# Kernel optimization log

Hardware: AMD Instinct MI355X
Metric: run time of the kernel (lower is better)

The kernel has to match this reference:

```python
import jax, jax.numpy as jnp
import numpy as np


def hadamard(D):
    # Sylvester Hadamard: H[i,j] = (-1)^popcount(i & j), normalized by sqrt(D)
    x = np.arange(D)[:, None] & np.arange(D)[None, :]
    par = np.zeros_like(x)
    for _ in range(int(np.log2(D)) + 1):
        par ^= x & 1
        x >>= 1
    return ((1.0 - 2.0 * par) / np.sqrt(D)).astype(np.float32)


def setup_inputs() -> dict:
    key = jax.random.key(0)
    ks = jax.random.split(key, 6)
    K, M, D, T = 4, 32, 2048, 128
    z = jax.random.normal(ks[0], (K, M, D, T), dtype=jnp.float32)
    d1 = jax.random.normal(ks[1], (D, 1), dtype=jnp.float32)
    d2 = jax.random.normal(ks[2], (D, 1), dtype=jnp.float32)
    d3 = jax.random.normal(ks[3], (D, 1), dtype=jnp.float32)
    b = jax.random.normal(ks[4], (D, 1), dtype=jnp.float32)
    sldj = jax.random.normal(ks[5], (K * M,), dtype=jnp.float32)
    return {"z": z, "d1": d1, "d2": d2, "d3": d3, "b": b,
            "sum_log_det_jacobians": sldj}


def reference(z, d1, d2, d3, b, sum_log_det_jacobians):
    K, M, D, T = z.shape
    H = jnp.asarray(hadamard(D), dtype=z.dtype)
    # A = H @ D3 @ H @ D2 @ H @ D1
    #   H @ diag(d)  == H * d.T (scale columns)
    #   diag(d) @ X  == d * X   (scale rows)
    A = H @ (d3 * (H @ (d2 * (H * d1[:, 0][None, :]))))
    # apply: tensordot(A, z, [[1],[2]]) then transpose to (K,M,D,T), add bias
    z_out = jnp.einsum('de,kmet->kmdt', A, z) + b[None, None, :, :]
    # log|det A| = sum_i log|d1_i| + log|d2_i| + log|d3_i|  (H is orthogonal)
    log_det_A = (jnp.sum(jnp.log(jnp.abs(d1)))
                 + jnp.sum(jnp.log(jnp.abs(d2)))
                 + jnp.sum(jnp.log(jnp.abs(d3))))
    sldj = sum_log_det_jacobians + log_det_A * jnp.ones((K * M,), dtype=z.dtype)
    return z_out, sldj
```

## Files before the change

kernel.cpp:

```cpp
#include <hip/hip_runtime.h>
#include <math.h>

#define D_DIM 2048
#define T_DIM 128
#define TT 16

__device__ __forceinline__ int sw1(int x) { return x ^ ((x >> 5) & 1); }
__device__ __forceinline__ int sw2(int x) { return x ^ ((x >> 4) & 1); }

#define BFLY(MM)                                              \
    _Pragma("unroll")                                         \
    for (int i_ = 0; i_ < 64; ++i_) {                         \
        if ((i_ & (MM)) == 0) {                               \
            float a_ = v[i_], b_ = v[i_ | (MM)];              \
            v[i_] = a_ + b_;                                  \
            v[i_ | (MM)] = a_ - b_;                           \
        }                                                     \
    }

__global__ __launch_bounds__(512, 4)
void fwht_apply_kernel(const float* __restrict__ z,
                       const float* __restrict__ d1,
                       const float* __restrict__ d2,
                       const float* __restrict__ d3,
                       const float* __restrict__ bvec,
                       float* __restrict__ out) {
    __shared__ float lds[1024 * TT];
    const int tid = threadIdx.x;
    const int r   = tid >> 4;
    const int tt  = tid & 15;
    const int bid = blockIdx.x;
    const int km  = bid >> 3;
    const int t0  = (bid & 7) << 4;
    const float s = 0.022097086912079608f;

    const float* zb = z + ((size_t)km * D_DIM) * T_DIM + t0 + tt;
    float v[64];

    #pragma unroll
    for (int j = 0; j < 64; ++j) {
        const int e = (j << 5) | r;
        v[j] = zb[(size_t)e * T_DIM] * (d1[e] * s);
    }
    BFLY(1) BFLY(2) BFLY(4) BFLY(8) BFLY(16) BFLY(32)

    #pragma unroll
    for (int j = 0; j < 32; ++j)
        lds[sw1((j << 5) | r) * TT + tt] = v[j];
    __syncthreads();
    #pragma unroll
    for (int j = 0; j < 32; ++j)
        v[j] = lds[sw1(j | (r << 5)) * TT + tt];
    __syncthreads();
    #pragma unroll
    for (int j = 32; j < 64; ++j)
        lds[sw1(((j & 31) << 5) | r) * TT + tt] = v[j];
    __syncthreads();
    #pragma unroll
    for (int j = 32; j < 64; ++j)
        v[j] = lds[sw1((j & 31) | (r << 5)) * TT + tt];
    __syncthreads();

    BFLY(1) BFLY(2) BFLY(4) BFLY(8) BFLY(16)
    {
        const float4* q0 = (const float4*)(d2 + (r << 5));
        const float4* q1 = (const float4*)(d2 + 1024 + (r << 5));
        #pragma unroll
        for (int q = 0; q < 8; ++q) {
            float4 a = q0[q];
            v[4*q+0] *= a.x * s; v[4*q+1] *= a.y * s;
            v[4*q+2] *= a.z * s; v[4*q+3] *= a.w * s;
            float4 c = q1[q];
            v[32+4*q+0] *= c.x * s; v[32+4*q+1] *= c.y * s;
            v[32+4*q+2] *= c.z * s; v[32+4*q+3] *= c.w * s;
        }
    }
    BFLY(1) BFLY(2) BFLY(4) BFLY(8) BFLY(16) BFLY(32)

    #pragma unroll
    for (int j = 0; j < 64; j += 2)
        lds[sw2(((j >> 1) & 15) | (r << 4) | ((j >> 5) << 9)) * TT + tt] = v[j];
    __syncthreads();
    #pragma unroll
    for (int j = 0; j < 64; j += 2)
        v[j] = lds[sw2((((j >> 1) & 31) << 4) | (r & 15) | ((r >> 4) << 9)) * TT + tt];
    __syncthreads();
    #pragma unroll
    for (int j = 1; j < 64; j += 2)
        lds[sw2(((j >> 1) & 15) | (r << 4) | ((j >> 5) << 9)) * TT + tt] = v[j];
    __syncthreads();
    #pragma unroll
    for (int j = 1; j < 64; j += 2)
        v[j] = lds[sw2((((j >> 1) & 31) << 4) | (r & 15) | ((r >> 4) << 9)) * TT + tt];
    __syncthreads();

    BFLY(2) BFLY(4) BFLY(8) BFLY(16) BFLY(32)
    {
        const int eRest = ((r & 15) << 1) | ((r >> 4) << 10);
        #pragma unroll
        for (int m = 0; m < 32; ++m) {
            float2 a = *(const float2*)(d3 + ((m << 5) | eRest));
            v[2*m]   *= a.x * s;
            v[2*m+1] *= a.y * s;
        }
    }
    BFLY(2) BFLY(4) BFLY(8) BFLY(16) BFLY(32) BFLY(1)

    #pragma unroll
    for (int j = 0; j < 64; j += 2)
        lds[sw2((((j >> 1) & 31) << 4) | (r & 15) | ((r >> 4) << 9)) * TT + tt] = v[j];
    __syncthreads();
    #pragma unroll
    for (int j = 0; j < 64; j += 2)
        v[j] = lds[sw2(((j >> 1) & 15) | (r << 4) | ((j >> 5) << 9)) * TT + tt];
    __syncthreads();
    #pragma unroll
    for (int j = 1; j < 64; j += 2)
        lds[sw2((((j >> 1) & 31) << 4) | (r & 15) | ((r >> 4) << 9)) * TT + tt] = v[j];
    __syncthreads();
    #pragma unroll
    for (int j = 1; j < 64; j += 2)
        v[j] = lds[sw2(((j >> 1) & 15) | (r << 4) | ((j >> 5) << 9)) * TT + tt];

    BFLY(2) BFLY(4) BFLY(8) BFLY(16) BFLY(32)

    float* ob = out + ((size_t)km * D_DIM) * T_DIM + t0 + tt;
    {
        const float4* q0 = (const float4*)(bvec + (r << 5));
        const float4* q1 = (const float4*)(bvec + 1024 + (r << 5));
        #pragma unroll
        for (int q = 0; q < 8; ++q) {
            float4 a = q0[q];
            const int e0 = (r << 5) + 4*q;
            ob[(size_t)(e0+0) * T_DIM] = v[4*q+0] + a.x;
            ob[(size_t)(e0+1) * T_DIM] = v[4*q+1] + a.y;
            ob[(size_t)(e0+2) * T_DIM] = v[4*q+2] + a.z;
            ob[(size_t)(e0+3) * T_DIM] = v[4*q+3] + a.w;
            float4 c = q1[q];
            const int e1 = 1024 + (r << 5) + 4*q;
            ob[(size_t)(e1+0) * T_DIM] = v[32+4*q+0] + c.x;
            ob[(size_t)(e1+1) * T_DIM] = v[32+4*q+1] + c.y;
            ob[(size_t)(e1+2) * T_DIM] = v[32+4*q+2] + c.z;
            ob[(size_t)(e1+3) * T_DIM] = v[32+4*q+3] + c.w;
        }
    }
}

__global__ void sldj_kernel(const float* __restrict__ d1,
                            const float* __restrict__ d2,
                            const float* __restrict__ d3,
                            const float* __restrict__ sldj_in,
                            float* __restrict__ out) {
    __shared__ float red[256];
    const int tid = threadIdx.x;
    float acc = 0.0f;
    for (int i = tid; i < D_DIM; i += 256) {
        acc += logf(fabsf(d1[i])) + logf(fabsf(d2[i])) + logf(fabsf(d3[i]));
    }
    red[tid] = acc;
    __syncthreads();
    #pragma unroll
    for (int sft = 128; sft > 0; sft >>= 1) {
        if (tid < sft) red[tid] += red[tid + sft];
        __syncthreads();
    }
    const float tot = red[0];
    if (tid < 128) out[tid] = sldj_in[tid] + tot;
}

extern "C" void kernel_launch(void* const* d_in, const int* in_sizes, int n_in,
                              void* d_out, int out_size, void* d_ws, size_t ws_size,
                              hipStream_t stream) {
    const float* z    = (const float*)d_in[0];
    const float* d1   = (const float*)d_in[1];
    const float* d2   = (const float*)d_in[2];
    const float* d3   = (const float*)d_in[3];
    const float* bvec = (const float*)d_in[4];
    const float* sldj = (const float*)d_in[5];
    float* out = (float*)d_out;

    fwht_apply_kernel<<<1024, 512, 0, stream>>>(z, d1, d2, d3, bvec, out);
    sldj_kernel<<<1, 256, 0, stream>>>(d1, d2, d3, sldj,
                                       out + (size_t)4 * 32 * 2048 * 128);
}
```

Measured before the change: 327.9 us.

## Stage z loads through LDS with float4 reads and fold sldj into main kernel

The initial load of z now uses coalesced float4 reads staged through LDS in two halves, replacing per-thread 4-byte strided global loads. The separate sldj reduction kernel is merged in as an extra block of the main grid, which removes one kernel launch. The launch-bounds occupancy hint drops from 4 to 2 blocks, which gives the compiler more registers but may reduce latency hiding. The staging adds two extra barriers and LDS round trips before the first butterfly.

```diff
diff --git a/kernel.cpp b/kernel.cpp
--- a/kernel.cpp
+++ b/kernel.cpp
@@ -18,15 +18,33 @@
         }                                                     \
     }
 
-__global__ __launch_bounds__(512, 4)
+__global__ __launch_bounds__(512, 2)
 void fwht_apply_kernel(const float* __restrict__ z,
                        const float* __restrict__ d1,
                        const float* __restrict__ d2,
                        const float* __restrict__ d3,
                        const float* __restrict__ bvec,
+                       const float* __restrict__ sldj_in,
                        float* __restrict__ out) {
     __shared__ float lds[1024 * TT];
     const int tid = threadIdx.x;
+
+    if (blockIdx.x == 1024) {
+        float acc = 0.0f;
+        for (int i = tid; i < D_DIM; i += 512)
+            acc += logf(fabsf(d1[i])) + logf(fabsf(d2[i])) + logf(fabsf(d3[i]));
+        lds[tid] = acc;
+        __syncthreads();
+        #pragma unroll
+        for (int sft = 256; sft > 0; sft >>= 1) {
+            if (tid < sft) lds[tid] += lds[tid + sft];
+            __syncthreads();
+        }
+        if (tid < 128)
+            out[(size_t)4 * 32 * 2048 * 128 + tid] = sldj_in[tid] + lds[0];
+        return;
+    }
+
     const int r   = tid >> 4;
     const int tt  = tid & 15;
     const int bid = blockIdx.x;
@@ -34,14 +52,34 @@
     const int t0  = (bid & 7) << 4;
     const float s = 0.022097086912079608f;
 
-    const float* zb = z + ((size_t)km * D_DIM) * T_DIM + t0 + tt;
+    const float* zslab = z + ((size_t)km << 18) + t0;
+    const int wid  = tid >> 6;
+    const int lane = tid & 63;
+    const int q    = lane >> 2;
+    const int c    = lane & 3;
+
     float v[64];
 
     #pragma unroll
-    for (int j = 0; j < 64; ++j) {
-        const int e = (j << 5) | r;
-        v[j] = zb[(size_t)e * T_DIM] * (d1[e] * s);
+    for (int h = 0; h < 2; ++h) {
+        #pragma unroll
+        for (int i = 0; i < 8; ++i) {
+            const int n = (wid << 3) | i;
+            const int e = (n << 5) | (h << 4) | q;
+            float4 tmp = *(const float4*)(zslab + (size_t)e * T_DIM + (c << 2));
+            ((float4*)lds)[(n << 6) + (q << 2) + c] = tmp;
+        }
+        __syncthreads();
+        if (((r >> 4) & 1) == h) {
+            #pragma unroll
+            for (int j = 0; j < 64; ++j) {
+                const int e = (j << 5) | r;
+                v[j] = lds[(((r & 15) | (j << 4)) << 4) + tt] * (d1[e] * s);
+            }
+        }
+        __syncthreads();
     }
+
     BFLY(1) BFLY(2) BFLY(4) BFLY(8) BFLY(16) BFLY(32)
 
     #pragma unroll
@@ -66,13 +104,13 @@
         const float4* q0 = (const float4*)(d2 + (r << 5));
         const float4* q1 = (const float4*)(d2 + 1024 + (r << 5));
         #pragma unroll
-        for (int q = 0; q < 8; ++q) {
-            float4 a = q0[q];
-            v[4*q+0] *= a.x * s; v[4*q+1] *= a.y * s;
-            v[4*q+2] *= a.z * s; v[4*q+3] *= a.w * s;
-            float4 c = q1[q];
-            v[32+4*q+0] *= c.x * s; v[32+4*q+1] *= c.y * s;
-            v[32+4*q+2] *= c.z * s; v[32+4*q+3] *= c.w * s;
+        for (int qq = 0; qq < 8; ++qq) {
+            float4 a = q0[qq];
+            v[4*qq+0] *= a.x * s; v[4*qq+1] *= a.y * s;
+            v[4*qq+2] *= a.z * s; v[4*qq+3] *= a.w * s;
+            float4 cc = q1[qq];
+            v[32+4*qq+0] *= cc.x * s; v[32+4*qq+1] *= cc.y * s;
+            v[32+4*qq+2] *= cc.z * s; v[32+4*qq+3] *= cc.w * s;
         }
     }
     BFLY(1) BFLY(2) BFLY(4) BFLY(8) BFLY(16) BFLY(32)
@@ -124,48 +162,26 @@
 
     BFLY(2) BFLY(4) BFLY(8) BFLY(16) BFLY(32)
 
-    float* ob = out + ((size_t)km * D_DIM) * T_DIM + t0 + tt;
+    float* ob = out + ((size_t)km << 18) + t0 + tt;
     {
         const float4* q0 = (const float4*)(bvec + (r << 5));
         const float4* q1 = (const float4*)(bvec + 1024 + (r << 5));
         #pragma unroll
-        for (int q = 0; q < 8; ++q) {
-            float4 a = q0[q];
-            const int e0 = (r << 5) + 4*q;
-            ob[(size_t)(e0+0) * T_DIM] = v[4*q+0] + a.x;
-            ob[(size_t)(e0+1) * T_DIM] = v[4*q+1] + a.y;
-            ob[(size_t)(e0+2) * T_DIM] = v[4*q+2] + a.z;
-            ob[(size_t)(e0+3) * T_DIM] = v[4*q+3] + a.w;
-            float4 c = q1[q];
-            const int e1 = 1024 + (r << 5) + 4*q;
-            ob[(size_t)(e1+0) * T_DIM] = v[32+4*q+0] + c.x;
-            ob[(size_t)(e1+1) * T_DIM] = v[32+4*q+1] + c.y;
-            ob[(size_t)(e1+2) * T_DIM] = v[32+4*q+2] + c.z;
-            ob[(size_t)(e1+3) * T_DIM] = v[32+4*q+3] + c.w;
+        for (int qq = 0; qq < 8; ++qq) {
+            float4 a = q0[qq];
+            const int e0 = (r << 5) + 4*qq;
+            ob[(size_t)(e0+0) * T_DIM] = v[4*qq+0] + a.x;
+            ob[(size_t)(e0+1) * T_DIM] = v[4*qq+1] + a.y;
+            ob[(size_t)(e0+2) * T_DIM] = v[4*qq+2] + a.z;
+            ob[(size_t)(e0+3) * T_DIM] = v[4*qq+3] + a.w;
+            float4 cc = q1[qq];
+            const int e1 = 1024 + (r << 5) + 4*qq;
+            ob[(size_t)(e1+0) * T_DIM] = v[32+4*qq+0] + cc.x;
+            ob[(size_t)(e1+1) * T_DIM] = v[32+4*qq+1] + cc.y;
+            ob[(size_t)(e1+2) * T_DIM] = v[32+4*qq+2] + cc.z;
+            ob[(size_t)(e1+3) * T_DIM] = v[32+4*qq+3] + cc.w;
         }
     }
-}
-
-__global__ void sldj_kernel(const float* __restrict__ d1,
-                            const float* __restrict__ d2,
-                            const float* __restrict__ d3,
-                            const float* __restrict__ sldj_in,
-                            float* __restrict__ out) {
-    __shared__ float red[256];
-    const int tid = threadIdx.x;
-    float acc = 0.0f;
-    for (int i = tid; i < D_DIM; i += 256) {
-        acc += logf(fabsf(d1[i])) + logf(fabsf(d2[i])) + logf(fabsf(d3[i]));
-    }
-    red[tid] = acc;
-    __syncthreads();
-    #pragma unroll
-    for (int sft = 128; sft > 0; sft >>= 1) {
-        if (tid < sft) red[tid] += red[tid + sft];
-        __syncthreads();
-    }
-    const float tot = red[0];
-    if (tid < 128) out[tid] = sldj_in[tid] + tot;
 }
 
 extern "C" void kernel_launch(void* const* d_in, const int* in_sizes, int n_in,
@@ -179,7 +195,5 @@
     const float* sldj = (const float*)d_in[5];
     float* out = (float*)d_out;
 
-    fwht_apply_kernel<<<1024, 512, 0, stream>>>(z, d1, d2, d3, bvec, out);
-    sldj_kernel<<<1, 256, 0, stream>>>(d1, d2, d3, sldj,
-                                       out + (size_t)4 * 32 * 2048 * 128);
+    fwht_apply_kernel<<<1025, 512, 0, stream>>>(z, d1, d2, d3, bvec, sldj, out);
 }
```

Result: faster. 302.4 us (-7.8%).
